# Optimization experiments

Measured on AMD Instinct MI355X. Metric: run time of the kernel, lower is better.

Reference implementation:

```python
import jax, jax.numpy as jnp
import numpy as np

B, S, H, NH = 2, 2048, 768, 12
HD = H // NH
MEM_W = 0.5  # memory_weight
LN_EPS = 1e-5


def setup_inputs() -> dict:
    key = jax.random.key(0)
    ks = jax.random.split(key, 12)
    xav = lambda k: jax.random.uniform(k, (H, H), jnp.float32, -1.0, 1.0) * np.sqrt(6.0 / (H + H))
    return {
        "hidden_states": jax.random.normal(ks[0], (B, S, H), jnp.float32),
        "cross_states": jax.random.normal(ks[1], (B, S, H), jnp.float32),
        "attention_mask": jnp.ones((B, 1, S, S), jnp.int32),
        "memory_tensors": jax.random.normal(ks[2], (2, B, S, H), jnp.float32),
        "dynamic_factor": jax.random.uniform(ks[3], (B, S, 1), jnp.float32),
        "Wq": xav(ks[4]), "bq": jnp.zeros((H,), jnp.float32),
        "Wk": xav(ks[5]), "bk": jnp.zeros((H,), jnp.float32),
        "Wv": xav(ks[6]), "bv": jnp.zeros((H,), jnp.float32),
        "Wo": xav(ks[7]), "bo": jnp.zeros((H,), jnp.float32),
        "gate": jnp.ones((1,), jnp.float32),
        "gate_bias": jnp.zeros((1,), jnp.float32),
        "ln_g": jnp.ones((H,), jnp.float32),
        "ln_b": jnp.zeros((H,), jnp.float32),
    }


def _layernorm(x, g, b):
    mu = jnp.mean(x, axis=-1, keepdims=True)
    var = jnp.mean(jnp.square(x - mu), axis=-1, keepdims=True)
    return (x - mu) * jax.lax.rsqrt(var + LN_EPS) * g + b


def reference(hidden_states, cross_states, attention_mask, memory_tensors,
              dynamic_factor, Wq, bq, Wk, bk, Wv, bv, Wo, bo,
              gate, gate_bias, ln_g, ln_b):
    x = _layernorm(hidden_states, ln_g, ln_b)
    q = x @ Wq + bq                      # [B,S,H]
    k = cross_states @ Wk + bk
    v = cross_states @ Wv + bv
    k = k + memory_tensors[0] * MEM_W    # memory injection into K/V
    v = v + memory_tensors[1] * MEM_W

    q = q.reshape(B, S, NH, HD).transpose(0, 2, 1, 3)  # [B,NH,S,HD]
    k = k.reshape(B, S, NH, HD).transpose(0, 2, 1, 3)
    v = v.reshape(B, S, NH, HD).transpose(0, 2, 1, 3)

    scores = jnp.einsum("bhqd,bhkd->bhqk", q, k) / np.sqrt(HD)
    scores = jnp.where(attention_mask == 0, -jnp.inf, scores)
    attn = jax.nn.softmax(scores, axis=-1)
    out = jnp.einsum("bhqk,bhkd->bhqd", attn, v)       # [B,NH,S,HD]
    out = out.transpose(0, 2, 1, 3).reshape(B, S, H)

    out = out @ Wo + bo
    out = out * gate + gate_bias
    out = out * dynamic_factor
    return out
```

## Files before the change

kernel.cpp:

```cpp
#include <hip/hip_runtime.h>
#include <hip/hip_bf16.h>
#include <stdint.h>

#define BB   2
#define SS   2048
#define HH   768
#define NHH  12
#define HDD  64
#define BSS  (BB*SS)
#define NBH  (BB*NHH)
#define ROWS_BH (NBH*SS)
#define NSPLIT 2

typedef unsigned short u16;
typedef unsigned int   u32;
typedef __attribute__((ext_vector_type(8))) short bf16x8_t;
typedef __attribute__((ext_vector_type(4))) float f32x4;
typedef __attribute__((ext_vector_type(2))) u32   u32x2;
typedef __attribute__((ext_vector_type(4))) u32   u32x4;

#define MFMA16(a, b, c) __builtin_amdgcn_mfma_f32_16x16x32_bf16((a), (b), (c), 0, 0, 0)

__device__ __forceinline__ float b2f(u16 u) {
    u32 x = ((u32)u) << 16; float f; __builtin_memcpy(&f, &x, 4); return f;
}
__device__ __forceinline__ u16 f2b(float f) {
    u32 x; __builtin_memcpy(&x, &f, 4);
    u32 r = x + 0x7fffu + ((x >> 16) & 1u);
    return (u16)(r >> 16);
}
__device__ __forceinline__ void async16(const u16* g, u16* l) {
    __builtin_amdgcn_global_load_lds(
        (const __attribute__((address_space(1))) void*)g,
        (__attribute__((address_space(3))) void*)l, 16, 0, 0);
}

__global__ __launch_bounds__(256) void prep_kernel(
    const float* __restrict__ Wq, const float* __restrict__ Wk,
    const float* __restrict__ Wv, const float* __restrict__ Wo,
    u16* __restrict__ Wt,
    const float* __restrict__ hid, const float* __restrict__ cross,
    const float* __restrict__ g, const float* __restrict__ bb,
    u16* __restrict__ xln, u16* __restrict__ crossb,
    const int* __restrict__ mask, u32* __restrict__ bits,
    u32* __restrict__ wrow)
{
    int id = blockIdx.x;
    int t = threadIdx.x;

    if (id < 576) {
        int mat = id / 144, rem = id % 144;
        int by = rem / 12, bx = rem % 12;
        const float* src = (mat == 0) ? Wq : (mat == 1) ? Wk : (mat == 2) ? Wv : Wo;
        u16* dst = Wt + (size_t)mat * 768 * 768;

        __shared__ float sm[64][68];
        int r0 = by * 64, c0 = bx * 64;
        #pragma unroll
        for (int it = 0; it < 4; ++it) {
            int c = t + it * 256;
            int r = c >> 4, sg = c & 15;
            *(float4*)&sm[r][sg * 4] = *(const float4*)&src[(size_t)(r0 + r) * 768 + c0 + sg * 4];
        }
        __syncthreads();
        #pragma unroll
        for (int it = 0; it < 2; ++it) {
            int c = t + it * 256;
            int rr = c >> 3, sg = c & 7;
            u16 tmp[8] __attribute__((aligned(16)));
            #pragma unroll
            for (int j = 0; j < 8; ++j) tmp[j] = f2b(sm[sg * 8 + j][rr]);
            *(u32x4*)&dst[(size_t)(c0 + rr) * 768 + r0 + sg * 8] = *(u32x4*)tmp;
        }
        return;
    }

    if (id < 2624) {
        int lid = id - 576;
        int y = lid >> 10, bx = lid & 1023;
        int wv = t >> 6, lane = t & 63;
        int row = bx * 4 + wv;

        if (y == 1) {
            const float* xr = cross + (size_t)row * 768;
            u16* o = crossb + (size_t)row * 768;
            #pragma unroll
            for (int c = 0; c < 3; ++c) {
                float4 f = *(const float4*)&xr[c * 256 + lane * 4];
                u16 t4[4] __attribute__((aligned(8)));
                t4[0] = f2b(f.x); t4[1] = f2b(f.y); t4[2] = f2b(f.z); t4[3] = f2b(f.w);
                *(u32x2*)&o[c * 256 + lane * 4] = *(u32x2*)t4;
            }
            return;
        }

        const float* xr = hid + (size_t)row * 768;
        float v[12];
        float s = 0.f, s2 = 0.f;
        #pragma unroll
        for (int c = 0; c < 3; ++c) {
            float4 f = *(const float4*)&xr[c * 256 + lane * 4];
            v[c*4+0] = f.x; v[c*4+1] = f.y; v[c*4+2] = f.z; v[c*4+3] = f.w;
            s  += f.x + f.y + f.z + f.w;
            s2 += f.x*f.x + f.y*f.y + f.z*f.z + f.w*f.w;
        }
        #pragma unroll
        for (int off = 1; off < 64; off <<= 1) {
            s  += __shfl_xor(s,  off, 64);
            s2 += __shfl_xor(s2, off, 64);
        }
        float mu  = s  * (1.f / 768.f);
        float var = s2 * (1.f / 768.f) - mu * mu;
        float rs  = 1.f / sqrtf(var + 1e-5f);
        #pragma unroll
        for (int c = 0; c < 3; ++c) {
            float4 gg = *(const float4*)&g [c * 256 + lane * 4];
            float4 bv = *(const float4*)&bb[c * 256 + lane * 4];
            u16 o[4] __attribute__((aligned(8)));
            o[0] = f2b((v[c*4+0] - mu) * rs * gg.x + bv.x);
            o[1] = f2b((v[c*4+1] - mu) * rs * gg.y + bv.y);
            o[2] = f2b((v[c*4+2] - mu) * rs * gg.z + bv.z);
            o[3] = f2b((v[c*4+3] - mu) * rs * gg.w + bv.w);
            *(u32x2*)&xln[(size_t)row * 768 + c * 256 + lane * 4] = *(u32x2*)o;
        }
        return;
    }

    {
        int mid = id - 2624;
        int w = mid * 256 + t;
        const int4* p = (const int4*)(mask + (size_t)w * 32);
        u32 v = 0;
        #pragma unroll
        for (int i = 0; i < 8; ++i) {
            int4 m = p[i];
            v |= ((m.x != 0) ? 1u : 0u) << (4 * i + 0);
            v |= ((m.y != 0) ? 1u : 0u) << (4 * i + 1);
            v |= ((m.z != 0) ? 1u : 0u) << (4 * i + 2);
            v |= ((m.w != 0) ? 1u : 0u) << (4 * i + 3);
        }
        bits[w] = v;
        unsigned long long ball = __ballot(v == 0xffffffffu);
        if ((t & 63) == 0) {
            u32 wr = 0;
            #pragma unroll
            for (int kt = 0; kt < 32; ++kt)
                if (((ball >> (2 * kt)) & 3ull) == 3ull) wr |= (1u << kt);
            wrow[w >> 6] = wr;
        }
    }
}

__device__ __forceinline__ void gemm128_main(const u16* __restrict__ A,
                                             const u16* __restrict__ W,
                                             f32x4 acc[4][4])
{
    __shared__ __attribute__((aligned(16))) u16 AsL[128 * 64];
    __shared__ __attribute__((aligned(16))) u16 BsL[128 * 64];
    int m0 = blockIdx.x * 128, n0 = blockIdx.y * 128;
    int t = threadIdx.x;
    int wv = t >> 6, lane = t & 63, lm = lane & 15, quad = lane >> 4;
    int wr = wv >> 1, wc = wv & 1;

    for (int kt = 0; kt < 768 / 64; ++kt) {
        __syncthreads();
        #pragma unroll
        for (int it = 0; it < 4; ++it) {
            int c = t + it * 256;
            int row = c >> 3, cs = (c & 7) ^ (row & 7);
            async16(A + (size_t)(m0 + row) * 768 + kt * 64 + cs * 8, &AsL[c * 8]);
            async16(W + (size_t)(n0 + row) * 768 + kt * 64 + cs * 8, &BsL[c * 8]);
        }
        __syncthreads();
        #pragma unroll
        for (int kk = 0; kk < 2; ++kk) {
            bf16x8_t af[4], bfv[4];
            #pragma unroll
            for (int i = 0; i < 4; ++i) {
                int r = wr * 64 + i * 16 + lm;
                af[i] = *(const bf16x8_t*)&AsL[(r * 8 + ((kk * 4 + quad) ^ (r & 7))) * 8];
            }
            #pragma unroll
            for (int j = 0; j < 4; ++j) {
                int r = wc * 64 + j * 16 + lm;
                bfv[j] = *(const bf16x8_t*)&BsL[(r * 8 + ((kk * 4 + quad) ^ (r & 7))) * 8];
            }
            #pragma unroll
            for (int i = 0; i < 4; ++i)
                #pragma unroll
                for (int j = 0; j < 4; ++j)
                    acc[i][j] = MFMA16(af[i], bfv[j], acc[i][j]);
        }
    }
}

__global__ __launch_bounds__(256) void qkv_gemm(
    const u16* __restrict__ xln, const u16* __restrict__ crossb,
    const u16* __restrict__ Wt,  const float* __restrict__ bq,
    const float* __restrict__ bk, const float* __restrict__ bv,
    const float* __restrict__ mem,
    u16* __restrict__ Qb, u16* __restrict__ Kb, u16* __restrict__ VtG)
{
    int z = blockIdx.z;
    const u16* A      = (z == 0) ? xln : crossb;
    const u16* W      = Wt + (size_t)z * 768 * 768;
    const float* bias = (z == 0) ? bq : (z == 1) ? bk : bv;
    const float* mp   = (z == 0) ? (const float*)nullptr : mem + (size_t)(z - 1) * BSS * HH;

    f32x4 z4 = {0.f, 0.f, 0.f, 0.f};
    f32x4 acc[4][4];
    #pragma unroll
    for (int i = 0; i < 4; ++i)
        #pragma unroll
        for (int j = 0; j < 4; ++j) acc[i][j] = z4;

    gemm128_main(A, W, acc);

    int t = threadIdx.x, wv = t >> 6, lane = t & 63, lm = lane & 15, quad = lane >> 4;
    int wr = wv >> 1, wc = wv & 1;
    int row0 = blockIdx.x * 128 + wr * 64 + quad * 4;
    int col0 = blockIdx.y * 128 + wc * 64 + lm;

    if (z == 2) {
        #pragma unroll
        for (int j = 0; j < 4; ++j) {
            int cg = col0 + j * 16;
            float bz = bias[cg];
            int h = cg >> 6, d = cg & 63;
            #pragma unroll
            for (int i = 0; i < 4; ++i) {
                int rg = row0 + i * 16;
                int b = rg >> 11, s = rg & 2047;
                u16 ob[4] __attribute__((aligned(8)));
                #pragma unroll
                for (int e = 0; e < 4; ++e) {
                    float v = acc[i][j][e] + bz + 0.5f * mp[(size_t)(rg + e) * HH + cg];
                    ob[e] = f2b(v);
                }
                *(u32x2*)&VtG[((size_t)(b * NHH + h) * 64 + d) * SS + s] = *(u32x2*)ob;
            }
        }
        return;
    }

    u16* out = (z == 0) ? Qb : Kb;
    #pragma unroll
    for (int j = 0; j < 4; ++j) {
        int cg = col0 + j * 16;
        float bz = bias[cg];
        #pragma unroll
        for (int i = 0; i < 4; ++i) {
            int rg = row0 + i * 16;
            #pragma unroll
            for (int e = 0; e < 4; ++e) {
                float v = acc[i][j][e] + bz;
                if (mp) v += 0.5f * mp[(size_t)(rg + e) * HH + cg];
                out[(size_t)(rg + e) * HH + cg] = f2b(v);
            }
        }
    }
}

__global__ __launch_bounds__(512) void attn_kernel(
    const u16* __restrict__ Q, const u16* __restrict__ K,
    const u16* __restrict__ VtG, const u32* __restrict__ mbits,
    const u32* __restrict__ wrow,
    u16* __restrict__ Pacc, float* __restrict__ Pl, int ksteps)
{
    __shared__ __attribute__((aligned(16))) u16   KsL[64 * 64];
    __shared__ __attribute__((aligned(16))) u16   VtL[64 * 64];
    __shared__ __attribute__((aligned(16))) short Ps[8][16][72];

    int qt = blockIdx.x;
    int bh = blockIdx.y;
    int z  = blockIdx.z;
    int b = bh / NHH, h = bh % NHH;
    int t = threadIdx.x;
    int wv = t >> 6, lane = t & 63, lm = lane & 15, quad = lane >> 4;
    int r7 = lm & 7;

    int qrow_g = b * SS + qt * 128 + wv * 16;
    const u16* qp = Q + (size_t)(qrow_g + lm) * HH + h * 64;
    bf16x8_t qf0 = *(const bf16x8_t*)&qp[quad * 8];
    bf16x8_t qf1 = *(const bf16x8_t*)&qp[32 + quad * 8];

    f32x4 z4 = {0.f, 0.f, 0.f, 0.f};
    f32x4 acc_o[4] = {z4, z4, z4, z4};
    float l_part[4] = {0.f, 0.f, 0.f, 0.f};

    const float SC = 0.18033688011112042f;
    int qloc = qt * 128 + wv * 16 + quad * 4;

    u32 wand = wrow[b * SS + qloc + 0] & wrow[b * SS + qloc + 1] &
               wrow[b * SS + qloc + 2] & wrow[b * SS + qloc + 3];

    int kr = t >> 3, cs = (t & 7) ^ (kr & 7);
    const u16* Kb0 = K + (size_t)(b * SS) * HH + h * 64;
    const u16* Vb0 = VtG + (size_t)bh * 64 * SS;

    int kt0 = z * ksteps;
    for (int kt = kt0; kt < kt0 + ksteps; ++kt) {
        __syncthreads();
        int k0 = kt * 64;
        async16(Kb0 + (size_t)(k0 + kr) * HH + cs * 8, &KsL[t * 8]);
        async16(Vb0 + (size_t)kr * SS + k0 + cs * 8,   &VtL[t * 8]);
        __syncthreads();

        f32x4 sc[4];
        #pragma unroll
        for (int k16 = 0; k16 < 4; ++k16) {
            int rowk = k16 * 16 + lm;
            bf16x8_t kf0 = *(const bf16x8_t*)&KsL[(rowk * 8 + (quad ^ r7)) * 8];
            bf16x8_t kf1 = *(const bf16x8_t*)&KsL[(rowk * 8 + ((quad ^ 4) ^ r7)) * 8];
            f32x4 a = z4;
            a = MFMA16(qf0, kf0, a);
            a = MFMA16(qf1, kf1, a);
            sc[k16] = a;
        }

        if (!__all((int)((wand >> kt) & 1u))) {
            #pragma unroll
            for (int e = 0; e < 4; ++e) {
                u32x2 u = *(const u32x2*)&mbits[(size_t)(b * SS + qloc + e) * (SS / 32) + kt * 2];
                unsigned long long mw = ((unsigned long long)u.y << 32) | (unsigned long long)u.x;
                #pragma unroll
                for (int k16 = 0; k16 < 4; ++k16)
                    if (!((mw >> (k16 * 16 + lm)) & 1ull)) sc[k16][e] = -3.0e38f;
            }
        }

        #pragma unroll
        for (int k16 = 0; k16 < 4; ++k16) {
            #pragma unroll
            for (int e = 0; e < 4; ++e) {
                float p = __builtin_amdgcn_exp2f(sc[k16][e] * SC);
                sc[k16][e] = p;
                l_part[e] += p;
            }
        }

        #pragma unroll
        for (int k16 = 0; k16 < 4; ++k16) {
            int colg = ((k16 + quad) & 3) * 16;
            #pragma unroll
            for (int e = 0; e < 4; ++e) {
                float pv = sc[k16][e];
                u32 pb = __builtin_bit_cast(u32, pv);
                Ps[wv][quad * 4 + e][colg + lm] = (short)((pb + 0x8000u) >> 16);
            }
        }
        __asm__ volatile("" ::: "memory");

        #pragma unroll
        for (int cc = 0; cc < 2; ++cc) {
            int k16r = cc * 2 + (quad >> 1);
            int colg = ((k16r + (lm >> 2)) & 3) * 16 + (quad & 1) * 8;
            bf16x8_t pf = *(const bf16x8_t*)&Ps[wv][lm][colg];
            #pragma unroll
            for (int j = 0; j < 4; ++j) {
                bf16x8_t vf = *(const bf16x8_t*)&VtL[((j * 16 + lm) * 8 + ((cc * 4 + quad) ^ r7)) * 8];
                acc_o[j] = MFMA16(pf, vf, acc_o[j]);
            }
        }
    }

    #pragma unroll
    for (int off = 1; off < 16; off <<= 1) {
        #pragma unroll
        for (int e = 0; e < 4; ++e)
            l_part[e] += __shfl_xor(l_part[e], off, 64);
    }

    size_t prow = ((size_t)z * NBH + bh) * SS + qt * 128 + wv * 16 + quad * 4;
    #pragma unroll
    for (int j = 0; j < 4; ++j)
        #pragma unroll
        for (int e = 0; e < 4; ++e)
            Pacc[(prow + e) * 64 + j * 16 + lm] = f2b(acc_o[j][e]);
    if (lm == 0) {
        #pragma unroll
        for (int e = 0; e < 4; ++e)
            Pl[prow + e] = l_part[e];
    }
}

__global__ __launch_bounds__(256) void attn_merge(
    const u16* __restrict__ Pacc, const float* __restrict__ Pl,
    u16* __restrict__ AO)
{
    int t = threadIdx.x;
    int r = blockIdx.x * 64 + (t >> 2);
    int dseg = (t & 3) * 16;

    float lsum = Pl[r] + Pl[(size_t)ROWS_BH + r];

    float o[16];
    #pragma unroll
    for (int i = 0; i < 16; ++i) o[i] = 0.f;
    #pragma unroll
    for (int s = 0; s < NSPLIT; ++s) {
        const u16* ap = &Pacc[((size_t)s * ROWS_BH + r) * 64 + dseg];
        u32x4 a0 = *(const u32x4*)ap;
        u32x4 a1 = *(const u32x4*)(ap + 8);
        u32 wa[8];
        wa[0]=a0.x; wa[1]=a0.y; wa[2]=a0.z; wa[3]=a0.w;
        wa[4]=a1.x; wa[5]=a1.y; wa[6]=a1.z; wa[7]=a1.w;
        #pragma unroll
        for (int i = 0; i < 8; ++i) {
            o[2*i]   += b2f((u16)(wa[i] & 0xffff));
            o[2*i+1] += b2f((u16)(wa[i] >> 16));
        }
    }
    float inv = 1.f / lsum;
    int bh = r >> 11, q = r & 2047;
    int b = bh / NHH, h = bh % NHH;
    u16 ob[16] __attribute__((aligned(16)));
    #pragma unroll
    for (int i = 0; i < 16; ++i) ob[i] = f2b(o[i] * inv);
    u16* op = &AO[((size_t)(b * SS + q)) * HH + h * 64 + dseg];
    *(u32x4*)op       = *(u32x4*)ob;
    *(u32x4*)(op + 8) = *(u32x4*)(ob + 8);
}

__global__ __launch_bounds__(256) void out_gemm(
    const u16* __restrict__ AO, const u16* __restrict__ Wt,
    const float* __restrict__ bo, const float* __restrict__ gate,
    const float* __restrict__ gbias, const float* __restrict__ dyn,
    float* __restrict__ out)
{
    f32x4 z4 = {0.f, 0.f, 0.f, 0.f};
    f32x4 acc[4][4];
    #pragma unroll
    for (int i = 0; i < 4; ++i)
        #pragma unroll
        for (int j = 0; j < 4; ++j) acc[i][j] = z4;

    gemm128_main(AO, Wt, acc);

    float gv = gate[0];
    float gb = gbias[0];
    int t = threadIdx.x, wv = t >> 6, lane = t & 63, lm = lane & 15, quad = lane >> 4;
    int wr = wv >> 1, wc = wv & 1;
    int row0 = blockIdx.x * 128 + wr * 64 + quad * 4;
    int col0 = blockIdx.y * 128 + wc * 64 + lm;
    #pragma unroll
    for (int j = 0; j < 4; ++j) {
        int cg = col0 + j * 16;
        float bz = bo[cg];
        #pragma unroll
        for (int i = 0; i < 4; ++i) {
            int rg = row0 + i * 16;
            #pragma unroll
            for (int e = 0; e < 4; ++e) {
                float v = acc[i][j][e] + bz;
                v = v * gv + gb;
                v *= dyn[rg + e];
                out[(size_t)(rg + e) * HH + cg] = v;
            }
        }
    }
}

extern "C" void kernel_launch(void* const* d_in, const int* in_sizes, int n_in,
                              void* d_out, int out_size, void* d_ws, size_t ws_size,
                              hipStream_t stream)
{
    (void)in_sizes; (void)n_in; (void)out_size; (void)ws_size;

    const float* hid   = (const float*)d_in[0];
    const float* cross = (const float*)d_in[1];
    const int*   amask = (const int*)d_in[2];
    const float* mem   = (const float*)d_in[3];
    const float* dyn   = (const float*)d_in[4];
    const float* Wq    = (const float*)d_in[5];
    const float* bq    = (const float*)d_in[6];
    const float* Wk    = (const float*)d_in[7];
    const float* bk    = (const float*)d_in[8];
    const float* Wv    = (const float*)d_in[9];
    const float* bv    = (const float*)d_in[10];
    const float* Wo    = (const float*)d_in[11];
    const float* bo    = (const float*)d_in[12];
    const float* gate  = (const float*)d_in[13];
    const float* gbias = (const float*)d_in[14];
    const float* lng   = (const float*)d_in[15];
    const float* lnb   = (const float*)d_in[16];

    char* p = (char*)d_ws;
    u16* Wt   = (u16*)p; p += (size_t)4 * 768 * 768 * 2;
    u32* mb   = (u32*)p; p += (size_t)BB * SS * (SS / 32) * 4;
    u32* wrow = (u32*)p; p += (size_t)BSS * 4;
    u16* xln  = (u16*)p; p += (size_t)BSS * HH * 2;
    u16* crb  = (u16*)p; p += (size_t)BSS * HH * 2;
    u16* Qb   = (u16*)p; p += (size_t)BSS * HH * 2;
    u16* Kb   = (u16*)p; p += (size_t)BSS * HH * 2;
    u16* VtG  = (u16*)p; p += (size_t)BSS * HH * 2;
    u16* Pacc  = xln;
    float* Pl  = (float*)Wt;
    u16* AO    = Kb;

    prep_kernel <<<dim3(3648),           256, 0, stream>>>(
        Wq, Wk, Wv, Wo, Wt, hid, cross, lng, lnb, xln, crb, amask, mb, wrow);
    qkv_gemm    <<<dim3(32, 6, 3),       256, 0, stream>>>(
        xln, crb, Wt, bq, bk, bv, mem, Qb, Kb, VtG);
    attn_kernel <<<dim3(16, 24, NSPLIT), 512, 0, stream>>>(
        Qb, Kb, VtG, mb, wrow, Pacc, Pl, SS / 64 / NSPLIT);
    attn_merge  <<<dim3(ROWS_BH / 64),   256, 0, stream>>>(Pacc, Pl, AO);
    out_gemm    <<<dim3(32, 6),          256, 0, stream>>>(
        AO, Wt + (size_t)3 * 768 * 768, bo, gate, gbias, dyn, (float*)d_out);
}
```

Before: 262.3 us.

## Double-buffer LDS tiles in QKV GEMM and attention loops

Both the projection GEMM main loop and the attention K/V loop now keep two shared-memory buffers. The next tile's async loads are issued before computing on the current tile, which removes one barrier per iteration and lets global loads overlap with MFMA work. This doubles the LDS footprint of both kernels, which may reduce occupancy. Correctness depends on async16 completing before the single end-of-iteration barrier; if async16 is a direct global-to-LDS load that needs an explicit vmcnt wait, the barrier alone may not be enough.

```diff
diff --git a/kernel.cpp b/kernel.cpp
--- a/kernel.cpp
+++ b/kernel.cpp
@@ -155,35 +155,41 @@
                                              const u16* __restrict__ W,
                                              f32x4 acc[4][4])
 {
-    __shared__ __attribute__((aligned(16))) u16 AsL[128 * 64];
-    __shared__ __attribute__((aligned(16))) u16 BsL[128 * 64];
+    __shared__ __attribute__((aligned(16))) u16 AsL[2][128 * 64];
+    __shared__ __attribute__((aligned(16))) u16 BsL[2][128 * 64];
     int m0 = blockIdx.x * 128, n0 = blockIdx.y * 128;
     int t = threadIdx.x;
     int wv = t >> 6, lane = t & 63, lm = lane & 15, quad = lane >> 4;
     int wr = wv >> 1, wc = wv & 1;
 
-    for (int kt = 0; kt < 768 / 64; ++kt) {
-        __syncthreads();
+    auto STAGE = [&](int pp, int kt) {
         #pragma unroll
         for (int it = 0; it < 4; ++it) {
             int c = t + it * 256;
             int row = c >> 3, cs = (c & 7) ^ (row & 7);
-            async16(A + (size_t)(m0 + row) * 768 + kt * 64 + cs * 8, &AsL[c * 8]);
-            async16(W + (size_t)(n0 + row) * 768 + kt * 64 + cs * 8, &BsL[c * 8]);
-        }
-        __syncthreads();
+            async16(A + (size_t)(m0 + row) * 768 + kt * 64 + cs * 8, &AsL[pp][c * 8]);
+            async16(W + (size_t)(n0 + row) * 768 + kt * 64 + cs * 8, &BsL[pp][c * 8]);
+        }
+    };
+
+    STAGE(0, 0);
+    __syncthreads();
+
+    for (int kt = 0; kt < 768 / 64; ++kt) {
+        int p = kt & 1;
+        if (kt < 768 / 64 - 1) STAGE(p ^ 1, kt + 1);
         #pragma unroll
         for (int kk = 0; kk < 2; ++kk) {
             bf16x8_t af[4], bfv[4];
             #pragma unroll
             for (int i = 0; i < 4; ++i) {
                 int r = wr * 64 + i * 16 + lm;
-                af[i] = *(const bf16x8_t*)&AsL[(r * 8 + ((kk * 4 + quad) ^ (r & 7))) * 8];
+                af[i] = *(const bf16x8_t*)&AsL[p][(r * 8 + ((kk * 4 + quad) ^ (r & 7))) * 8];
             }
             #pragma unroll
             for (int j = 0; j < 4; ++j) {
                 int r = wc * 64 + j * 16 + lm;
-                bfv[j] = *(const bf16x8_t*)&BsL[(r * 8 + ((kk * 4 + quad) ^ (r & 7))) * 8];
+                bfv[j] = *(const bf16x8_t*)&BsL[p][(r * 8 + ((kk * 4 + quad) ^ (r & 7))) * 8];
             }
             #pragma unroll
             for (int i = 0; i < 4; ++i)
@@ -191,6 +197,7 @@
                 for (int j = 0; j < 4; ++j)
                     acc[i][j] = MFMA16(af[i], bfv[j], acc[i][j]);
         }
+        __syncthreads();
     }
 }
 
@@ -267,8 +274,8 @@
     const u32* __restrict__ wrow,
     u16* __restrict__ Pacc, float* __restrict__ Pl, int ksteps)
 {
-    __shared__ __attribute__((aligned(16))) u16   KsL[64 * 64];
-    __shared__ __attribute__((aligned(16))) u16   VtL[64 * 64];
+    __shared__ __attribute__((aligned(16))) u16   KsL[2][64 * 64];
+    __shared__ __attribute__((aligned(16))) u16   VtL[2][64 * 64];
     __shared__ __attribute__((aligned(16))) short Ps[8][16][72];
 
     int qt = blockIdx.x;
@@ -298,20 +305,26 @@
     const u16* Kb0 = K + (size_t)(b * SS) * HH + h * 64;
     const u16* Vb0 = VtG + (size_t)bh * 64 * SS;
 
-    int kt0 = z * ksteps;
-    for (int kt = kt0; kt < kt0 + ksteps; ++kt) {
-        __syncthreads();
+    auto STAGE = [&](int pp, int kt) {
         int k0 = kt * 64;
-        async16(Kb0 + (size_t)(k0 + kr) * HH + cs * 8, &KsL[t * 8]);
-        async16(Vb0 + (size_t)kr * SS + k0 + cs * 8,   &VtL[t * 8]);
-        __syncthreads();
+        async16(Kb0 + (size_t)(k0 + kr) * HH + cs * 8, &KsL[pp][t * 8]);
+        async16(Vb0 + (size_t)kr * SS + k0 + cs * 8,   &VtL[pp][t * 8]);
+    };
+
+    int kt0 = z * ksteps, ktE = kt0 + ksteps;
+    STAGE(0, kt0);
+    __syncthreads();
+
+    for (int kt = kt0; kt < ktE; ++kt) {
+        int p = (kt - kt0) & 1;
+        if (kt + 1 < ktE) STAGE(p ^ 1, kt + 1);
 
         f32x4 sc[4];
         #pragma unroll
         for (int k16 = 0; k16 < 4; ++k16) {
             int rowk = k16 * 16 + lm;
-            bf16x8_t kf0 = *(const bf16x8_t*)&KsL[(rowk * 8 + (quad ^ r7)) * 8];
-            bf16x8_t kf1 = *(const bf16x8_t*)&KsL[(rowk * 8 + ((quad ^ 4) ^ r7)) * 8];
+            bf16x8_t kf0 = *(const bf16x8_t*)&KsL[p][(rowk * 8 + (quad ^ r7)) * 8];
+            bf16x8_t kf1 = *(const bf16x8_t*)&KsL[p][(rowk * 8 + ((quad ^ 4) ^ r7)) * 8];
             f32x4 a = z4;
             a = MFMA16(qf0, kf0, a);
             a = MFMA16(qf1, kf1, a);
@@ -333,9 +346,9 @@
         for (int k16 = 0; k16 < 4; ++k16) {
             #pragma unroll
             for (int e = 0; e < 4; ++e) {
-                float p = __builtin_amdgcn_exp2f(sc[k16][e] * SC);
-                sc[k16][e] = p;
-                l_part[e] += p;
+                float pv = __builtin_amdgcn_exp2f(sc[k16][e] * SC);
+                sc[k16][e] = pv;
+                l_part[e] += pv;
             }
         }
 
@@ -358,10 +371,12 @@
             bf16x8_t pf = *(const bf16x8_t*)&Ps[wv][lm][colg];
             #pragma unroll
             for (int j = 0; j < 4; ++j) {
-                bf16x8_t vf = *(const bf16x8_t*)&VtL[((j * 16 + lm) * 8 + ((cc * 4 + quad) ^ r7)) * 8];
+                bf16x8_t vf = *(const bf16x8_t*)&VtL[p][((j * 16 + lm) * 8 + ((cc * 4 + quad) ^ r7)) * 8];
                 acc_o[j] = MFMA16(pf, vf, acc_o[j]);
             }
         }
+
+        __syncthreads();
     }
 
     #pragma unroll
```

After: 261.2 us. About the same (-0.4%).
